# Kernel optimization log

Hardware: AMD Instinct MI355X
Metric: run time of the kernel (lower is better)

## Reference

```python
import jax, jax.numpy as jnp
import numpy as np

B, N, C, K, RANK, NLAYERS = 16, 8192, 64, 128, 4, 4
NDIM, IN_DIM = 2, 3

def _modes():
    kx, ky = np.meshgrid(np.arange(16), np.arange(8), indexing='ij')
    kp = np.stack([kx.ravel(), ky.ravel()], axis=-1).astype(np.float32)  # [128, 2]
    return jnp.asarray(2.0 * np.pi * kp)  # k_pairs / Ls with Ls=[1,1]

def setup_inputs() -> dict:
    key = jax.random.key(0)
    ks = jax.random.split(key, 16)
    feats = jax.random.normal(ks[0], (B, N, IN_DIM), dtype=jnp.float32)
    grid = jax.random.uniform(ks[1], (B, N, NDIM), dtype=jnp.float32)
    weights = jnp.full((B, N, 1), 1.0 / N, dtype=jnp.float32)
    mask = jnp.ones((B, N, 1), dtype=jnp.float32)
    x = jnp.concatenate([feats, grid, weights, mask], axis=-1)  # [B, N, 7]
    s1 = 1.0 / (C * np.sqrt(RANK))
    s2 = 1.0 / (C * np.sqrt(RANK))
    return {
        'x': x,
        'fc0_w': 0.1 * jax.random.normal(ks[2], (IN_DIM, C), dtype=jnp.float32),
        'fc0_b': jnp.zeros((C,), dtype=jnp.float32),
        'wc1': s1 * jax.random.uniform(ks[3], (NLAYERS, C, RANK, K), dtype=jnp.float32),
        'wc2': s2 * jax.random.uniform(ks[4], (NLAYERS, RANK, C, K), dtype=jnp.float32),
        'ws1': s1 * jax.random.uniform(ks[5], (NLAYERS, C, RANK, K), dtype=jnp.float32),
        'ws2': s2 * jax.random.uniform(ks[6], (NLAYERS, RANK, C, K), dtype=jnp.float32),
        'w01': s1 * jax.random.uniform(ks[7], (NLAYERS, C, RANK, 1), dtype=jnp.float32),
        'w02': s2 * jax.random.uniform(ks[8], (NLAYERS, RANK, C, 1), dtype=jnp.float32),
        'wconv': 0.05 * jax.random.normal(ks[9], (NLAYERS, C, C), dtype=jnp.float32),
        'bconv': jnp.zeros((NLAYERS, C), dtype=jnp.float32),
        'fc1_w': 0.1 * jax.random.normal(ks[10], (C, 128), dtype=jnp.float32),
        'fc1_b': jnp.zeros((128,), dtype=jnp.float32),
        'fc2_w': 0.1 * jax.random.normal(ks[11], (128, 1), dtype=jnp.float32),
        'fc2_b': jnp.zeros((1,), dtype=jnp.float32),
    }

def _lowrank(xh, w1, w2):
    # xh: [b,i,k]; w1: [i,r,k]; w2: [r,o,k] -> [b,o,k]
    return jnp.einsum('brk,rok->bok', jnp.einsum('bik,irk->brk', xh, w1), w2)

def reference(x, fc0_w, fc0_b, wc1, wc2, ws1, ws2, w01, w02, wconv, bconv, fc1_w, fc1_b, fc2_w, fc2_b):
    modes = _modes()  # [K, NDIM]
    aux = jnp.transpose(x[..., -(2 + NDIM):], (0, 2, 1))  # [B, 4, N]
    grid, weights, mask = aux[:, :NDIM], aux[:, -2:-1], aux[:, -1:]
    size = grid.shape[-1]
    temp = jnp.einsum('bdx,kd->bkx', grid, modes)  # [B, K, N]
    bases_c = jnp.cos(temp) * mask
    bases_s = jnp.sin(temp) * mask
    bases_0 = mask  # [B, 1, N]
    wsz = weights * size
    wbases_c, wbases_s, wbases_0 = bases_c * wsz, bases_s * wsz, bases_0 * wsz

    h = x[..., :IN_DIM] @ fc0_w + fc0_b  # [B, N, C]
    h = jnp.transpose(h, (0, 2, 1))      # [B, C, N]
    inv_sqrt = 1.0 / jnp.sqrt(jnp.float32(size))

    for i in range(NLAYERS):
        x_c = jnp.einsum('bix,bkx->bik', h, wbases_c)
        x_s = -jnp.einsum('bix,bkx->bik', h, wbases_s)
        x_0 = jnp.einsum('bix,bkx->bik', h, wbases_0)
        c1, c2 = wc1[i] * inv_sqrt, wc2[i] * inv_sqrt
        s1, s2 = ws1[i] * inv_sqrt, ws2[i] * inv_sqrt
        z1, z2 = w01[i] * inv_sqrt, w02[i] * inv_sqrt
        f_c = _lowrank(x_c, c1, c2) - _lowrank(x_s, s1, s2)
        f_s = _lowrank(x_s, c1, c2) + _lowrank(x_c, s1, s2)
        f_0 = _lowrank(x_0, z1, z2)
        x1 = (jnp.einsum('bok,bkx->box', f_0, bases_0)
              + 2.0 * jnp.einsum('bok,bkx->box', f_c, bases_c)
              - 2.0 * jnp.einsum('bok,bkx->box', f_s, bases_s))
        x2 = jnp.einsum('bix,io->box', h, wconv[i]) + bconv[i][None, :, None]
        h = x1 + x2
        if i != NLAYERS - 1:
            h = jax.nn.gelu(h, approximate=False)

    out = jnp.transpose(h, (0, 2, 1))  # [B, N, C]
    out = jax.nn.gelu(out @ fc1_w + fc1_b, approximate=False)
    out = out @ fc2_w + fc2_b  # [B, N, 1]
    return out
```

## Files before the change

### kernel.cpp

```cpp
#include <hip/hip_runtime.h>
#include <math.h>

namespace {
constexpr int cB = 16, cN = 8192, cC = 64, cK = 128, cR = 4, cNL = 4;
constexpr float kTwoPi = 6.28318530717958647692f;

constexpr size_t OFF_H     = 0;
constexpr size_t OFF_PACKA = (size_t)cB * cC * cN;
constexpr size_t OFF_PACKB = OFF_PACKA + (size_t)cB * cN * 4;
constexpr size_t OFF_PACKC = OFF_PACKB + (size_t)cB * cN * 4;
constexpr size_t OFF_PC    = OFF_PACKC + (size_t)cB * cN * 2;
constexpr size_t OFF_PS    = OFF_PC + (size_t)512 * 8192;
constexpr size_t OFF_XC    = OFF_PS + (size_t)512 * 8192;
constexpr size_t OFF_XS    = OFF_XC + (size_t)cB * cC * cK;
constexpr size_t OFF_FAH   = OFF_XS + (size_t)cB * cC * cK;
constexpr size_t OFF_FAL   = OFF_FAH + (size_t)cB * cC * 320 / 2;
constexpr size_t OFF_F0    = OFF_FAL + (size_t)cB * cC * 320 / 2;
constexpr size_t OFF_FW    = OFF_F0 + (size_t)cB * cC;

typedef _Float16 f16x8 __attribute__((ext_vector_type(8)));
typedef _Float16 f16x4 __attribute__((ext_vector_type(4)));
typedef float f32x4 __attribute__((ext_vector_type(4)));

__device__ __forceinline__ float gelu_f(float x) {
  return 0.5f * x * (1.0f + erff(x * 0.7071067811865475244f));
}

struct cpx { float x, y; };
__device__ __forceinline__ cpx cmul(cpx a, cpx b) {
  cpx r;
  r.x = fmaf(a.x, b.x, -(a.y * b.y));
  r.y = fmaf(a.x, b.y, a.y * b.x);
  return r;
}

__device__ __forceinline__ void split16(float v, _Float16& hi, _Float16& lo) {
  hi = (_Float16)v;
  lo = (_Float16)((v - (float)hi) * 1024.0f);
}
}

__global__ void __launch_bounds__(256) k_prep(const float* __restrict__ x,
                                              const float* __restrict__ fc0_w,
                                              const float* __restrict__ fc0_b,
                                              float* __restrict__ ws) {
  int t = blockIdx.x * 256 + threadIdx.x;
  int b = t >> 13;
  int n = t & (cN - 1);
  const float* xp = x + (size_t)t * 7;
  float f0 = xp[0], f1 = xp[1], f2 = xp[2];
  float gx = xp[3], gy = xp[4], w = xp[5], m = xp[6];
  float ax = kTwoPi * gx, ay = kTwoPi * gy;
  float sx, cx, sy, cy, s8x, c8x, s4y, c4y;
  sincosf(ax, &sx, &cx);
  sincosf(ay, &sy, &cy);
  sincosf(8.0f * ax, &s8x, &c8x);
  sincosf(4.0f * ay, &s4y, &c4y);
  ((float4*)(ws + OFF_PACKA))[t] = make_float4(cx, sx, cy, sy);
  ((float4*)(ws + OFF_PACKB))[t] = make_float4(c8x, s8x, c4y, s4y);
  ((float2*)(ws + OFF_PACKC))[t] = make_float2(w * (float)cN * m, m);
  float* h = ws + OFF_H + (size_t)b * cC * cN + n;
#pragma unroll
  for (int c = 0; c < cC; c++) {
    float v = fc0_b[c] + f0 * fc0_w[c] + f1 * fc0_w[cC + c] + f2 * fc0_w[2 * cC + c];
    h[(size_t)c * cN] = v;
  }
}

__global__ void k_prepw(const float* __restrict__ fc1_w, float* __restrict__ ws) {
  int j = threadIdx.x;
  _Float16* FWh = (_Float16*)(ws + OFF_FW);
  _Float16* FWl = FWh + 128 * 64;
  for (int c = 0; c < cC; c++) {
    _Float16 hi, lo;
    split16(fc1_w[c * 128 + j], hi, lo);
    FWh[j * 64 + c] = hi;
    FWl[j * 64 + c] = lo;
  }
}

__global__ void __launch_bounds__(256, 2) k_forward(const float* __restrict__ hg,
                                                    const float* __restrict__ ws,
                                                    float* __restrict__ Pc,
                                                    float* __restrict__ Ps) {
  __shared__ __align__(16) _Float16 lAh[64 * 40];
  __shared__ __align__(16) _Float16 lAl[64 * 40];
  __shared__ __align__(16) _Float16 lWh[256 * 40];
  __shared__ __align__(16) _Float16 lWl[256 * 40];
  int b = blockIdx.y, nb = blockIdx.x;
  int n_base = nb * 256;
  int tid = threadIdx.x;
  int lane = tid & 63, w = tid >> 6;
  int l15 = lane & 15, quad = lane >> 4;
  int sc = tid & 63, skg = tid >> 6;
  int mg = tid >> 3, pg = tid & 7;
  int kx = mg >> 1, ky0 = (mg & 1) * 4;
  const float4* pA = (const float4*)(ws + OFF_PACKA) + (size_t)b * cN;
  const float4* pB = (const float4*)(ws + OFF_PACKB) + (size_t)b * cN;
  const float2* pC = (const float2*)(ws + OFF_PACKC) + (size_t)b * cN;
  const float* hb = hg + (size_t)b * cC * cN;
  f32x4 acc0[4][4], acc1[4][4];
  f32x4 zz = {0.0f, 0.0f, 0.0f, 0.0f};
#pragma unroll
  for (int i = 0; i < 4; i++)
#pragma unroll
    for (int j = 0; j < 4; j++) { acc0[i][j] = zz; acc1[i][j] = zz; }

  for (int s = 0; s < 8; s++) {
    int n0 = n_base + s * 32;
    {
      const float* hrow = hb + (size_t)sc * cN + n0 + skg * 8;
      float4 va = *(const float4*)hrow;
      float4 vb = *(const float4*)(hrow + 4);
      float vals[8] = {va.x, va.y, va.z, va.w, vb.x, vb.y, vb.z, vb.w};
      f16x8 hi8, lo8;
#pragma unroll
      for (int e = 0; e < 8; e++) {
        _Float16 hv, lv;
        split16(vals[e], hv, lv);
        hi8[e] = hv;
        lo8[e] = lv;
      }
      *(f16x8*)&lAh[sc * 40 + skg * 8] = hi8;
      *(f16x8*)&lAl[sc * 40 + skg * 8] = lo8;
    }
    {
      _Float16 chi[4][4], clo[4][4], shi[4][4], slo[4][4];
#pragma unroll
      for (int q = 0; q < 4; q++) {
        int p = n0 + pg * 4 + q;
        float4 a4 = pA[p];
        float4 b4 = pB[p];
        float wsz = pC[p].x;
        cpx ex{a4.x, a4.y}, ey{a4.z, a4.w}, ex8{b4.x, b4.y}, ey4{b4.z, b4.w};
        cpx ex2 = cmul(ex, ex);
        cpx ex4v = cmul(ex2, ex2);
        cpx u{wsz, 0.0f};
        if (kx & 1) u = cmul(u, ex);
        if (kx & 2) u = cmul(u, ex2);
        if (kx & 4) u = cmul(u, ex4v);
        if (kx & 8) u = cmul(u, ex8);
        cpx v;
        if (ky0) v = ey4; else v = cpx{1.0f, 0.0f};
#pragma unroll
        for (int j = 0; j < 4; j++) {
          cpx m = cmul(u, v);
          split16(m.x, chi[j][q], clo[j][q]);
          split16(m.y, shi[j][q], slo[j][q]);
          v = cmul(v, ey);
        }
      }
      int mbase = kx * 8 + ky0;
#pragma unroll
      for (int j = 0; j < 4; j++) {
        int mc = mbase + j, ms = 128 + mbase + j;
        f16x4 t0 = {chi[j][0], chi[j][1], chi[j][2], chi[j][3]};
        f16x4 t1 = {clo[j][0], clo[j][1], clo[j][2], clo[j][3]};
        f16x4 t2 = {shi[j][0], shi[j][1], shi[j][2], shi[j][3]};
        f16x4 t3 = {slo[j][0], slo[j][1], slo[j][2], slo[j][3]};
        *(f16x4*)&lWh[mc * 40 + pg * 4] = t0;
        *(f16x4*)&lWl[mc * 40 + pg * 4] = t1;
        *(f16x4*)&lWh[ms * 40 + pg * 4] = t2;
        *(f16x4*)&lWl[ms * 40 + pg * 4] = t3;
      }
    }
    __syncthreads();
    f16x8 Ahf[4], Alf[4];
#pragma unroll
    for (int mt = 0; mt < 4; mt++) {
      Ahf[mt] = *(const f16x8*)&lAh[(mt * 16 + l15) * 40 + quad * 8];
      Alf[mt] = *(const f16x8*)&lAl[(mt * 16 + l15) * 40 + quad * 8];
    }
#pragma unroll
    for (int nt = 0; nt < 4; nt++) {
      int row = w * 64 + nt * 16 + l15;
      f16x8 Bh = *(const f16x8*)&lWh[row * 40 + quad * 8];
      f16x8 Bl = *(const f16x8*)&lWl[row * 40 + quad * 8];
#pragma unroll
      for (int mt = 0; mt < 4; mt++) {
        acc0[mt][nt] = __builtin_amdgcn_mfma_f32_16x16x32_f16(Ahf[mt], Bh, acc0[mt][nt], 0, 0, 0);
        acc1[mt][nt] = __builtin_amdgcn_mfma_f32_16x16x32_f16(Ahf[mt], Bl, acc1[mt][nt], 0, 0, 0);
        acc1[mt][nt] = __builtin_amdgcn_mfma_f32_16x16x32_f16(Alf[mt], Bh, acc1[mt][nt], 0, 0, 0);
      }
    }
    __syncthreads();
  }
  float* pcb = Pc + (size_t)(b * 32 + nb) * 8192;
  float* psb = Ps + (size_t)(b * 32 + nb) * 8192;
  const float inv1024 = 1.0f / 1024.0f;
#pragma unroll
  for (int mt = 0; mt < 4; mt++)
#pragma unroll
    for (int nt = 0; nt < 4; nt++) {
      int nn = w * 64 + nt * 16 + l15;
      float* dst = (nn < 128) ? pcb : psb;
      int col = nn & 127;
#pragma unroll
      for (int r = 0; r < 4; r++) {
        int c = mt * 16 + quad * 4 + r;
        dst[c * 128 + col] = acc0[mt][nt][r] + acc1[mt][nt][r] * inv1024;
      }
    }
}

__global__ void __launch_bounds__(256) k_reduce(const float* __restrict__ Pc,
                                                const float* __restrict__ Ps,
                                                float* __restrict__ Xc,
                                                float* __restrict__ Xs) {
  int idx = blockIdx.x * 256 + threadIdx.x;
  int b = idx >> 13;
  int rest = idx & 8191;
  float sc = 0.0f, ss = 0.0f;
#pragma unroll
  for (int nb = 0; nb < 32; nb++) {
    sc += Pc[(size_t)(b * 32 + nb) * 8192 + rest];
    ss += Ps[(size_t)(b * 32 + nb) * 8192 + rest];
  }
  Xc[idx] = sc;
  Xs[idx] = ss;
}

__global__ void __launch_bounds__(64) k_lowrank(const float* __restrict__ Xc,
                                                const float* __restrict__ Xs,
                                                const float* __restrict__ wc1,
                                                const float* __restrict__ wc2,
                                                const float* __restrict__ ws1,
                                                const float* __restrict__ ws2,
                                                const float* __restrict__ w01,
                                                const float* __restrict__ w02,
                                                const float* __restrict__ wconv,
                                                float* __restrict__ ws, int layer) {
  int b = blockIdx.x;
  int k = blockIdx.y;
  int tid = threadIdx.x;
  const float* xcb = Xc + (size_t)b * cC * cK;
  const float* xsb = Xs + (size_t)b * cC * cK;
  float xcv = xcb[(size_t)tid * cK + k];
  float xsv = -xsb[(size_t)tid * cK + k];
  const float* c1 = wc1 + (size_t)layer * cC * cR * cK + (size_t)tid * cR * cK + k;
  const float* s1 = ws1 + (size_t)layer * cC * cR * cK + (size_t)tid * cR * cK + k;
  float A1[cR], A2[cR], B1[cR], B2[cR];
#pragma unroll
  for (int r = 0; r < cR; r++) {
    float w1c = c1[(size_t)r * cK];
    float w1sv = s1[(size_t)r * cK];
    A1[r] = xcv * w1c;
    A2[r] = xcv * w1sv;
    B1[r] = xsv * w1c;
    B2[r] = xsv * w1sv;
  }
#pragma unroll
  for (int r = 0; r < cR; r++) {
#pragma unroll
    for (int off = 32; off > 0; off >>= 1) {
      A1[r] += __shfl_xor(A1[r], off);
      A2[r] += __shfl_xor(A2[r], off);
      B1[r] += __shfl_xor(B1[r], off);
      B2[r] += __shfl_xor(B2[r], off);
    }
  }
  const float scale = 2.0f / (float)cN;
  const float* c2 = wc2 + (size_t)layer * cR * cC * cK;
  const float* s2 = ws2 + (size_t)layer * cR * cC * cK;
  int o = tid;
  float fc = 0.0f, fs = 0.0f;
#pragma unroll
  for (int r = 0; r < cR; r++) {
    float w2c = c2[((size_t)r * cC + o) * cK + k];
    float w2s = s2[((size_t)r * cC + o) * cK + k];
    fc += A1[r] * w2c - B2[r] * w2s;
    fs += B1[r] * w2c + A2[r] * w2s;
  }
  _Float16* FAh = (_Float16*)(ws + OFF_FAH);
  _Float16* FAl = (_Float16*)(ws + OFF_FAL);
  size_t abase = ((size_t)b * cC + o) * 320;
  int rowc = ((k >> 5) << 6) + (k & 31);
  float vc = scale * fc;
  float vs = -scale * fs;
  _Float16 hi, lo;
  split16(vc, hi, lo);
  FAh[abase + rowc] = hi;
  FAl[abase + rowc] = lo;
  split16(vs, hi, lo);
  FAh[abase + rowc + 32] = hi;
  FAl[abase + rowc + 32] = lo;
  if (k < 64) {
    float wv = wconv[(size_t)layer * 4096 + (size_t)k * cC + o];
    split16(wv, hi, lo);
    FAh[abase + 256 + k] = hi;
    FAl[abase + 256 + k] = lo;
  }
  if (k == 0) {
    float t0[cR];
#pragma unroll
    for (int r = 0; r < cR; r++)
      t0[r] = xcv * w01[((size_t)layer * cC + tid) * cR + r];
#pragma unroll
    for (int r = 0; r < cR; r++) {
#pragma unroll
      for (int off = 32; off > 0; off >>= 1) t0[r] += __shfl_xor(t0[r], off);
    }
    float f = 0.0f;
#pragma unroll
    for (int r = 0; r < cR; r++) f += t0[r] * w02[((size_t)layer * cR + r) * cC + o];
    (ws + OFF_F0)[b * cC + o] = f / (float)cN;
  }
}

__global__ void __launch_bounds__(256, 3) k_inverse(float* __restrict__ h,
                                                    const float* __restrict__ ws,
                                                    const float* __restrict__ bconv,
                                                    int layer, int do_gelu) {
  __shared__ __align__(16) _Float16 lAh[2][64 * 36];
  __shared__ __align__(16) _Float16 lAl[2][64 * 36];
  __shared__ __align__(16) _Float16 lBh[2][64 * 36];
  __shared__ __align__(16) _Float16 lBl[2][64 * 36];
  int b = blockIdx.y;
  int n_blk = blockIdx.x * 64;
  int tid = threadIdx.x;
  int lane = tid & 63, w = tid >> 6;
  int l15 = lane & 15, quad = lane >> 4;
  int p = tid >> 2, sub = tid & 3;
  const float4* pA = (const float4*)(ws + OFF_PACKA) + (size_t)b * cN;
  const float4* pB = (const float4*)(ws + OFF_PACKB) + (size_t)b * cN;
  const float2* pC = (const float2*)(ws + OFF_PACKC) + (size_t)b * cN;
  float4 a4 = pA[n_blk + p];
  float4 b4 = pB[n_blk + p];
  float mval_p = pC[n_blk + p].y;
  cpx ex{a4.x, a4.y}, ey{a4.z, a4.w}, ex8{b4.x, b4.y}, ey4{b4.z, b4.w};
  cpx ex2 = cmul(ex, ex);
  cpx ex3 = cmul(ex2, ex);
  cpx ex4v = cmul(ex2, ex2);
  cpx ex12 = cmul(ex8, ex4v);
  cpx eyp[8];
  eyp[0] = {1.0f, 0.0f};
  eyp[1] = ey;
  eyp[2] = cmul(ey, ey);
  eyp[3] = cmul(eyp[2], ey);
  eyp[4] = ey4;
  eyp[5] = cmul(ey4, ey);
  eyp[6] = cmul(ey4, eyp[2]);
  eyp[7] = cmul(ey4, eyp[3]);
  int ncol = n_blk + w * 16 + l15;
  float mcol = pC[ncol].y;
  float* hb = h + (size_t)b * cC * cN;
  f16x8 cBh[2], cBl[2];
#pragma unroll
  for (int t = 0; t < 2; t++) {
#pragma unroll
    for (int j = 0; j < 8; j++) {
      int i = t * 32 + quad * 8 + j;
      float v = hb[(size_t)i * cN + ncol];
      _Float16 hi, lo;
      split16(v, hi, lo);
      cBh[t][j] = hi;
      cBl[t][j] = lo;
    }
  }
  const _Float16* FAh = (const _Float16*)(ws + OFF_FAH) + ((size_t)b * cC + p) * 320 + sub * 8;
  const _Float16* FAl = (const _Float16*)(ws + OFF_FAL) + ((size_t)b * cC + p) * 320 + sub * 8;
  f16x8 pf_h0 = *(const f16x8*)(FAh);
  f16x8 pf_h1 = *(const f16x8*)(FAh + 32);
  f16x8 pf_l0 = *(const f16x8*)(FAl);
  f16x8 pf_l1 = *(const f16x8*)(FAl + 32);
  f32x4 acc0[4], acc1[4];
  f32x4 zz = {0.0f, 0.0f, 0.0f, 0.0f};
#pragma unroll
  for (int i = 0; i < 4; i++) { acc0[i] = zz; acc1[i] = zz; }
  for (int sc = 0; sc < 5; sc++) {
    __syncthreads();
    *(f16x8*)&lAh[0][p * 36 + sub * 8] = pf_h0;
    *(f16x8*)&lAh[1][p * 36 + sub * 8] = pf_h1;
    *(f16x8*)&lAl[0][p * 36 + sub * 8] = pf_l0;
    *(f16x8*)&lAl[1][p * 36 + sub * 8] = pf_l1;
    if (sc < 4) {
      cpx base;
      if (sc == 0) base = cpx{1.0f, 0.0f};
      else if (sc == 1) base = ex4v;
      else if (sc == 2) base = ex8;
      else base = ex12;
      cpx u;
      if (sub == 0) u = base;
      else if (sub == 1) u = cmul(base, ex);
      else if (sub == 2) u = cmul(base, ex2);
      else u = cmul(base, ex3);
      u.x *= mval_p;
      u.y *= mval_p;
      f16x8 ch, cl, sh, sl;
#pragma unroll
      for (int ky = 0; ky < 8; ky++) {
        cpx m = cmul(u, eyp[ky]);
        _Float16 hi, lo;
        split16(m.x, hi, lo);
        ch[ky] = hi; cl[ky] = lo;
        split16(m.y, hi, lo);
        sh[ky] = hi; sl[ky] = lo;
      }
      *(f16x8*)&lBh[0][p * 36 + sub * 8] = ch;
      *(f16x8*)&lBl[0][p * 36 + sub * 8] = cl;
      *(f16x8*)&lBh[1][p * 36 + sub * 8] = sh;
      *(f16x8*)&lBl[1][p * 36 + sub * 8] = sl;
    }
    __syncthreads();
    if (sc < 4) {
      int koff = (sc + 1) * 64;
      pf_h0 = *(const f16x8*)(FAh + koff);
      pf_h1 = *(const f16x8*)(FAh + koff + 32);
      pf_l0 = *(const f16x8*)(FAl + koff);
      pf_l1 = *(const f16x8*)(FAl + koff + 32);
    }
#pragma unroll
    for (int t = 0; t < 2; t++) {
      f16x8 Af_h[4], Af_l[4];
#pragma unroll
      for (int mt = 0; mt < 4; mt++) {
        Af_h[mt] = *(const f16x8*)&lAh[t][(mt * 16 + l15) * 36 + quad * 8];
        Af_l[mt] = *(const f16x8*)&lAl[t][(mt * 16 + l15) * 36 + quad * 8];
      }
      f16x8 Bf_h, Bf_l;
      if (sc < 4) {
        Bf_h = *(const f16x8*)&lBh[t][(w * 16 + l15) * 36 + quad * 8];
        Bf_l = *(const f16x8*)&lBl[t][(w * 16 + l15) * 36 + quad * 8];
      } else {
        Bf_h = cBh[t];
        Bf_l = cBl[t];
      }
#pragma unroll
      for (int mt = 0; mt < 4; mt++) {
        acc0[mt] = __builtin_amdgcn_mfma_f32_16x16x32_f16(Af_h[mt], Bf_h, acc0[mt], 0, 0, 0);
        acc1[mt] = __builtin_amdgcn_mfma_f32_16x16x32_f16(Af_h[mt], Bf_l, acc1[mt], 0, 0, 0);
        acc1[mt] = __builtin_amdgcn_mfma_f32_16x16x32_f16(Af_l[mt], Bf_h, acc1[mt], 0, 0, 0);
      }
    }
  }
  const float* F0B = ws + OFF_F0 + (size_t)b * cC;
  const float inv1024 = 1.0f / 1024.0f;
#pragma unroll
  for (int mt = 0; mt < 4; mt++) {
#pragma unroll
    for (int r = 0; r < 4; r++) {
      int row = mt * 16 + quad * 4 + r;
      float v = acc0[mt][r] + acc1[mt][r] * inv1024 + F0B[row] * mcol +
                bconv[layer * cC + row];
      if (do_gelu) v = gelu_f(v);
      hb[(size_t)row * cN + ncol] = v;
    }
  }
}

__global__ void __launch_bounds__(256, 2) k_final(const float* __restrict__ h,
                                                  const float* __restrict__ ws,
                                                  const float* __restrict__ fc1_b,
                                                  const float* __restrict__ fc2_w,
                                                  const float* __restrict__ fc2_b,
                                                  float* __restrict__ out) {
  __shared__ __align__(16) _Float16 lFh[128 * 68];
  __shared__ __align__(16) _Float16 lFl[128 * 68];
  int b = blockIdx.y;
  int n_blk = blockIdx.x * 64;
  int tid = threadIdx.x;
  int lane = tid & 63, w = tid >> 6;
  int l15 = lane & 15, quad = lane >> 4;
  {
    const _Float16* FWh = (const _Float16*)(ws + OFF_FW);
    const _Float16* FWl = FWh + 128 * 64;
    int row = tid & 127, which = tid >> 7;
    const _Float16* src = (which ? FWl : FWh) + row * 64;
    _Float16* dst = (which ? lFl : lFh) + row * 68;
#pragma unroll
    for (int i = 0; i < 8; i++)
      *(f16x8*)&dst[i * 8] = *(const f16x8*)&src[i * 8];
  }
  int ncol = n_blk + w * 16 + l15;
  const float* hb = h + (size_t)b * cC * cN;
  f16x8 hBh[2], hBl[2];
#pragma unroll
  for (int t = 0; t < 2; t++) {
#pragma unroll
    for (int j = 0; j < 8; j++) {
      int c = t * 32 + quad * 8 + j;
      float v = hb[(size_t)c * cN + ncol];
      _Float16 hi, lo;
      split16(v, hi, lo);
      hBh[t][j] = hi;
      hBl[t][j] = lo;
    }
  }
  __syncthreads();
  f32x4 acc0[8], acc1[8];
  f32x4 zz = {0.0f, 0.0f, 0.0f, 0.0f};
#pragma unroll
  for (int i = 0; i < 8; i++) { acc0[i] = zz; acc1[i] = zz; }
#pragma unroll
  for (int t = 0; t < 2; t++) {
#pragma unroll
    for (int mt = 0; mt < 8; mt++) {
      f16x8 Ah = *(const f16x8*)&lFh[(mt * 16 + l15) * 68 + t * 32 + quad * 8];
      f16x8 Al = *(const f16x8*)&lFl[(mt * 16 + l15) * 68 + t * 32 + quad * 8];
      acc0[mt] = __builtin_amdgcn_mfma_f32_16x16x32_f16(Ah, hBh[t], acc0[mt], 0, 0, 0);
      acc1[mt] = __builtin_amdgcn_mfma_f32_16x16x32_f16(Ah, hBl[t], acc1[mt], 0, 0, 0);
      acc1[mt] = __builtin_amdgcn_mfma_f32_16x16x32_f16(Al, hBh[t], acc1[mt], 0, 0, 0);
    }
  }
  const float inv1024 = 1.0f / 1024.0f;
  float s = 0.0f;
#pragma unroll
  for (int mt = 0; mt < 8; mt++) {
#pragma unroll
    for (int r = 0; r < 4; r++) {
      int j = mt * 16 + quad * 4 + r;
      float t1 = acc0[mt][r] + acc1[mt][r] * inv1024 + fc1_b[j];
      s += gelu_f(t1) * fc2_w[j];
    }
  }
  s += __shfl_xor(s, 16);
  s += __shfl_xor(s, 32);
  if (quad == 0) out[(size_t)b * cN + ncol] = s + fc2_b[0];
}

extern "C" void kernel_launch(void* const* d_in, const int* in_sizes, int n_in,
                              void* d_out, int out_size, void* d_ws, size_t ws_size,
                              hipStream_t stream) {
  const float* x = (const float*)d_in[0];
  const float* fc0_w = (const float*)d_in[1];
  const float* fc0_b = (const float*)d_in[2];
  const float* wc1 = (const float*)d_in[3];
  const float* wc2 = (const float*)d_in[4];
  const float* ws1 = (const float*)d_in[5];
  const float* ws2 = (const float*)d_in[6];
  const float* w01 = (const float*)d_in[7];
  const float* w02 = (const float*)d_in[8];
  const float* wconv = (const float*)d_in[9];
  const float* bconv = (const float*)d_in[10];
  const float* fc1_w = (const float*)d_in[11];
  const float* fc1_b = (const float*)d_in[12];
  const float* fc2_w = (const float*)d_in[13];
  const float* fc2_b = (const float*)d_in[14];
  float* ws = (float*)d_ws;
  float* out = (float*)d_out;
  float* h = ws + OFF_H;

  hipLaunchKernelGGL(k_prep, dim3(cB * cN / 256), dim3(256), 0, stream, x, fc0_w, fc0_b, ws);
  hipLaunchKernelGGL(k_prepw, dim3(1), dim3(128), 0, stream, fc1_w, ws);
  for (int l = 0; l < cNL; l++) {
    hipLaunchKernelGGL(k_forward, dim3(32, cB), dim3(256), 0, stream, h, ws,
                       ws + OFF_PC, ws + OFF_PS);
    hipLaunchKernelGGL(k_reduce, dim3(512), dim3(256), 0, stream,
                       ws + OFF_PC, ws + OFF_PS, ws + OFF_XC, ws + OFF_XS);
    hipLaunchKernelGGL(k_lowrank, dim3(cB, cK), dim3(64), 0, stream, ws + OFF_XC,
                       ws + OFF_XS, wc1, wc2, ws1, ws2, w01, w02, wconv, ws, l);
    hipLaunchKernelGGL(k_inverse, dim3(cN / 64, cB), dim3(256), 0, stream, h, ws,
                       bconv, l, (l != cNL - 1) ? 1 : 0);
  }
  hipLaunchKernelGGL(k_final, dim3(cN / 64, cB), dim3(256), 0, stream, h, ws,
                     fc1_b, fc2_w, fc2_b, out);
}
```

Before: 474.2 us.

## Prefetch next tile in forward DFT kernel, shrink LDS pad, merge prep launches

In k_forward, the global loads of the basis pack data and h rows for the next 32-point step are issued into registers right after the barrier, so they overlap the MFMA work of the current step. The barrier moves to the top of the loop. The LDS row stride drops from 40 to 36 halves, which changes bank mapping and LDS footprint. The separate fc1 weight-split kernel is folded into an extra block of k_prep, saving one launch. The price is higher register pressure from the prefetch buffers, and the 36 stride may bring in bank conflicts or misaligned 16-byte LDS accesses.

```diff
diff --git a/kernel.cpp b/kernel.cpp
--- a/kernel.cpp
+++ b/kernel.cpp
@@ -43,7 +43,22 @@
 __global__ void __launch_bounds__(256) k_prep(const float* __restrict__ x,
                                               const float* __restrict__ fc0_w,
                                               const float* __restrict__ fc0_b,
+                                              const float* __restrict__ fc1_w,
                                               float* __restrict__ ws) {
+  if (blockIdx.x == (unsigned)(cB * cN / 256)) {
+    int j = threadIdx.x;
+    if (j < 128) {
+      _Float16* FWh = (_Float16*)(ws + OFF_FW);
+      _Float16* FWl = FWh + 128 * 64;
+      for (int c = 0; c < cC; c++) {
+        _Float16 hi, lo;
+        split16(fc1_w[c * 128 + j], hi, lo);
+        FWh[j * 64 + c] = hi;
+        FWl[j * 64 + c] = lo;
+      }
+    }
+    return;
+  }
   int t = blockIdx.x * 256 + threadIdx.x;
   int b = t >> 13;
   int n = t & (cN - 1);
@@ -67,26 +82,14 @@
   }
 }
 
-__global__ void k_prepw(const float* __restrict__ fc1_w, float* __restrict__ ws) {
-  int j = threadIdx.x;
-  _Float16* FWh = (_Float16*)(ws + OFF_FW);
-  _Float16* FWl = FWh + 128 * 64;
-  for (int c = 0; c < cC; c++) {
-    _Float16 hi, lo;
-    split16(fc1_w[c * 128 + j], hi, lo);
-    FWh[j * 64 + c] = hi;
-    FWl[j * 64 + c] = lo;
-  }
-}
-
 __global__ void __launch_bounds__(256, 2) k_forward(const float* __restrict__ hg,
                                                     const float* __restrict__ ws,
                                                     float* __restrict__ Pc,
                                                     float* __restrict__ Ps) {
-  __shared__ __align__(16) _Float16 lAh[64 * 40];
-  __shared__ __align__(16) _Float16 lAl[64 * 40];
-  __shared__ __align__(16) _Float16 lWh[256 * 40];
-  __shared__ __align__(16) _Float16 lWl[256 * 40];
+  __shared__ __align__(16) _Float16 lAh[64 * 36];
+  __shared__ __align__(16) _Float16 lAl[64 * 36];
+  __shared__ __align__(16) _Float16 lWh[256 * 36];
+  __shared__ __align__(16) _Float16 lWl[256 * 36];
   int b = blockIdx.y, nb = blockIdx.x;
   int n_base = nb * 256;
   int tid = threadIdx.x;
@@ -106,13 +109,27 @@
 #pragma unroll
     for (int j = 0; j < 4; j++) { acc0[i][j] = zz; acc1[i][j] = zz; }
 
+  float4 pfA[4], pfB[4];
+  float pfW[4];
+  float4 pfh0, pfh1;
+  {
+    int n0 = n_base;
+#pragma unroll
+    for (int q = 0; q < 4; q++) {
+      int p = n0 + pg * 4 + q;
+      pfA[q] = pA[p];
+      pfB[q] = pB[p];
+      pfW[q] = pC[p].x;
+    }
+    const float* hrow = hb + (size_t)sc * cN + n0 + skg * 8;
+    pfh0 = *(const float4*)hrow;
+    pfh1 = *(const float4*)(hrow + 4);
+  }
   for (int s = 0; s < 8; s++) {
     int n0 = n_base + s * 32;
+    __syncthreads();
     {
-      const float* hrow = hb + (size_t)sc * cN + n0 + skg * 8;
-      float4 va = *(const float4*)hrow;
-      float4 vb = *(const float4*)(hrow + 4);
-      float vals[8] = {va.x, va.y, va.z, va.w, vb.x, vb.y, vb.z, vb.w};
+      float vals[8] = {pfh0.x, pfh0.y, pfh0.z, pfh0.w, pfh1.x, pfh1.y, pfh1.z, pfh1.w};
       f16x8 hi8, lo8;
 #pragma unroll
       for (int e = 0; e < 8; e++) {
@@ -121,17 +138,16 @@
         hi8[e] = hv;
         lo8[e] = lv;
       }
-      *(f16x8*)&lAh[sc * 40 + skg * 8] = hi8;
-      *(f16x8*)&lAl[sc * 40 + skg * 8] = lo8;
+      *(f16x8*)&lAh[sc * 36 + skg * 8] = hi8;
+      *(f16x8*)&lAl[sc * 36 + skg * 8] = lo8;
     }
     {
       _Float16 chi[4][4], clo[4][4], shi[4][4], slo[4][4];
 #pragma unroll
       for (int q = 0; q < 4; q++) {
-        int p = n0 + pg * 4 + q;
-        float4 a4 = pA[p];
-        float4 b4 = pB[p];
-        float wsz = pC[p].x;
+        float4 a4 = pfA[q];
+        float4 b4 = pfB[q];
+        float wsz = pfW[q];
         cpx ex{a4.x, a4.y}, ey{a4.z, a4.w}, ex8{b4.x, b4.y}, ey4{b4.z, b4.w};
         cpx ex2 = cmul(ex, ex);
         cpx ex4v = cmul(ex2, ex2);
@@ -158,24 +174,37 @@
         f16x4 t1 = {clo[j][0], clo[j][1], clo[j][2], clo[j][3]};
         f16x4 t2 = {shi[j][0], shi[j][1], shi[j][2], shi[j][3]};
         f16x4 t3 = {slo[j][0], slo[j][1], slo[j][2], slo[j][3]};
-        *(f16x4*)&lWh[mc * 40 + pg * 4] = t0;
-        *(f16x4*)&lWl[mc * 40 + pg * 4] = t1;
-        *(f16x4*)&lWh[ms * 40 + pg * 4] = t2;
-        *(f16x4*)&lWl[ms * 40 + pg * 4] = t3;
+        *(f16x4*)&lWh[mc * 36 + pg * 4] = t0;
+        *(f16x4*)&lWl[mc * 36 + pg * 4] = t1;
+        *(f16x4*)&lWh[ms * 36 + pg * 4] = t2;
+        *(f16x4*)&lWl[ms * 36 + pg * 4] = t3;
       }
     }
     __syncthreads();
+    if (s < 7) {
+      int n1 = n0 + 32;
+#pragma unroll
+      for (int q = 0; q < 4; q++) {
+        int p = n1 + pg * 4 + q;
+        pfA[q] = pA[p];
+        pfB[q] = pB[p];
+        pfW[q] = pC[p].x;
+      }
+      const float* hrow = hb + (size_t)sc * cN + n1 + skg * 8;
+      pfh0 = *(const float4*)hrow;
+      pfh1 = *(const float4*)(hrow + 4);
+    }
     f16x8 Ahf[4], Alf[4];
 #pragma unroll
     for (int mt = 0; mt < 4; mt++) {
-      Ahf[mt] = *(const f16x8*)&lAh[(mt * 16 + l15) * 40 + quad * 8];
-      Alf[mt] = *(const f16x8*)&lAl[(mt * 16 + l15) * 40 + quad * 8];
+      Ahf[mt] = *(const f16x8*)&lAh[(mt * 16 + l15) * 36 + quad * 8];
+      Alf[mt] = *(const f16x8*)&lAl[(mt * 16 + l15) * 36 + quad * 8];
     }
 #pragma unroll
     for (int nt = 0; nt < 4; nt++) {
       int row = w * 64 + nt * 16 + l15;
-      f16x8 Bh = *(const f16x8*)&lWh[row * 40 + quad * 8];
-      f16x8 Bl = *(const f16x8*)&lWl[row * 40 + quad * 8];
+      f16x8 Bh = *(const f16x8*)&lWh[row * 36 + quad * 8];
+      f16x8 Bl = *(const f16x8*)&lWl[row * 36 + quad * 8];
 #pragma unroll
       for (int mt = 0; mt < 4; mt++) {
         acc0[mt][nt] = __builtin_amdgcn_mfma_f32_16x16x32_f16(Ahf[mt], Bh, acc0[mt][nt], 0, 0, 0);
@@ -183,7 +212,6 @@
         acc1[mt][nt] = __builtin_amdgcn_mfma_f32_16x16x32_f16(Alf[mt], Bh, acc1[mt][nt], 0, 0, 0);
       }
     }
-    __syncthreads();
   }
   float* pcb = Pc + (size_t)(b * 32 + nb) * 8192;
   float* psb = Ps + (size_t)(b * 32 + nb) * 8192;
@@ -540,8 +568,8 @@
   float* out = (float*)d_out;
   float* h = ws + OFF_H;
 
-  hipLaunchKernelGGL(k_prep, dim3(cB * cN / 256), dim3(256), 0, stream, x, fc0_w, fc0_b, ws);
-  hipLaunchKernelGGL(k_prepw, dim3(1), dim3(128), 0, stream, fc1_w, ws);
+  hipLaunchKernelGGL(k_prep, dim3(cB * cN / 256 + 1), dim3(256), 0, stream, x, fc0_w,
+                     fc0_b, fc1_w, ws);
   for (int l = 0; l < cNL; l++) {
     hipLaunchKernelGGL(k_forward, dim3(32, cB), dim3(256), 0, stream, h, ws,
                        ws + OFF_PC, ws + OFF_PS);
```

New measurement: 475.3 us. No clear change (+0.2%).
